# Kernel optimization log

Measured on AMD Instinct MI355X. Metric: run time of the kernel, lower is better.

## Reference

```python
import jax, jax.numpy as jnp
import numpy as np

N = 500_000
E = 5_000_000
DIM = 16
LR = 0.005
THRESHOLD = 0.0


def setup_inputs() -> dict:
    key = jax.random.key(0)
    ks = jax.random.split(key, 8)
    s = 1.0 / np.sqrt(DIM)
    return {
        "x": jax.random.normal(ks[0], (N, DIM), jnp.float32),
        "edge_index": jax.random.randint(ks[1], (2, E), 0, N, dtype=jnp.int32),
        "W1": jax.random.normal(ks[2], (DIM, DIM), jnp.float32) * s,
        "b1": jnp.zeros((DIM,), jnp.float32),
        "W2": jax.random.normal(ks[3], (DIM, DIM), jnp.float32) * s,
        "b2": jnp.zeros((DIM,), jnp.float32),
        "W3": jax.random.normal(ks[4], (DIM, DIM), jnp.float32) * s,
        "b3": jnp.zeros((DIM,), jnp.float32),
        "positive": 0,  # negative sample -> nonzero loss branch
    }


def gcn_conv(x, edge_index, W, b):
    # PyG GCNConv: h = x @ W.T, add self-loops, symmetric norm, aggregate at dst.
    n = x.shape[0]
    loop = jnp.arange(n, dtype=edge_index.dtype)
    src = jnp.concatenate([edge_index[0], loop])
    dst = jnp.concatenate([edge_index[1], loop])
    deg = jax.ops.segment_sum(jnp.ones_like(dst, x.dtype), dst, num_segments=n)
    dinv = jnp.where(deg > 0, jax.lax.rsqrt(deg), 0.0)
    norm = dinv[src] * dinv[dst]  # [E+N]
    h = x @ W.T  # [N, out]
    msg = norm[:, None] * h[src]  # irregular gather, memory-bound
    return jax.ops.segment_sum(msg, dst, num_segments=n) + b


def local_loss(g, positive):
    t = THRESHOLD
    if positive:
        return jnp.where(g > t + 10.0, 0.0,
               jnp.where(g < t - 10.0, t - g, jnp.log1p(jnp.exp(t - g))))
    return jnp.where(g > t + 10.0, t + g,
           jnp.where(g < t - 10.0, 0.0, jnp.log1p(jnp.exp(g + t))))


def reference(x, edge_index, W1, b1, W2, b2, W3, b3, positive):
    # Note: the original computes activation_normalizer(x) and loss_derivative(g)
    # into z/driv_loss but immediately overwrites both -> dead code, omitted.
    agg = jnp.float32(0.0)
    Wc, bc = W1, b1  # conv1 params, updated in-place each layer in the original
    x_cur = x
    for (W, b) in ((W1, b1), (W2, b2), (W3, b3)):
        z = jax.nn.relu(gcn_conv(x_cur, edge_index, W, b))
        goodness = jnp.sum(z * z) / z.shape[1]
        agg = agg + local_loss(goodness, positive)
        d = 2.0 * jnp.abs(z)            # activation_gradient(z)
        wd = d * d                      # weighted_deriv
        dW = x_cur.T @ wd               # [in, out]
        db = jnp.sum(wd, axis=0)
        Wc = Wc - LR * dW.T
        bc = bc - LR * db
        x_cur = z
    return agg, Wc, bc
```

## Files before the change

kernel.cpp:

```cpp
#include <hip/hip_runtime.h>
#include <math.h>

#define TPB 256
#define TPB_P 512
#define TPB_A 512
#define LRATE 0.005f

#define LOG_NPB 10
#define NPB (1 << LOG_NPB)
#define CAP 14336
#define CHUNK 4096
#define CPT (CHUNK / TPB_P)

#define NTILE 64

#define FXS  65536.0f
#define FXSI (1.0f / 65536.0f)

#if __has_builtin(__builtin_amdgcn_cvt_f32_fp8) && __has_builtin(__builtin_amdgcn_cvt_pk_fp8_f32)
__device__ __forceinline__ float fp8_dec(unsigned char v) {
    return __builtin_amdgcn_cvt_f32_fp8((int)v, 0);
}
__device__ __forceinline__ unsigned fp8_pk4(float a, float b, float c, float d) {
    int w = __builtin_amdgcn_cvt_pk_fp8_f32(a, b, 0, false);
    w = __builtin_amdgcn_cvt_pk_fp8_f32(c, d, w, true);
    return (unsigned)w;
}
#else
__device__ __forceinline__ unsigned char fp8_enc1(float f) {
    unsigned u = __float_as_uint(f);
    unsigned s = (u >> 24) & 0x80u;
    u &= 0x7FFFFFFFu;
    if (u >= 0x43E00000u) return (unsigned char)(s | 0x7E);
    if (u < 0x3C800000u) {
        float a = __uint_as_float(u);
        int m = (int)rintf(a * 512.f);
        return (unsigned char)(s | (unsigned)m);
    }
    unsigned mant = u & 0x7FFFFFu;
    unsigned rest = mant & 0xFFFFFu;
    unsigned keep = u >> 20;
    keep += (rest > 0x80000u || (rest == 0x80000u && (keep & 1u))) ? 1u : 0u;
    int eb = (int)(keep >> 3) - 127 + 7;
    return (unsigned char)(s | (unsigned)((eb << 3) | (int)(keep & 7u)));
}
__device__ __forceinline__ float fp8_dec(unsigned char v) {
    unsigned s = ((unsigned)(v & 0x80u)) << 24;
    unsigned e = (v >> 3) & 0xFu;
    unsigned m = v & 7u;
    if (e == 0) {
        float r = (float)m * 0.001953125f;
        return (v & 0x80u) ? -r : r;
    }
    return __uint_as_float(s | ((e + 120u) << 23) | (m << 20));
}
__device__ __forceinline__ unsigned fp8_pk4(float a, float b, float c, float d) {
    return (unsigned)fp8_enc1(a) | ((unsigned)fp8_enc1(b) << 8) |
           ((unsigned)fp8_enc1(c) << 16) | ((unsigned)fp8_enc1(d) << 24);
}
#endif

#if __has_builtin(__builtin_amdgcn_cvt_pk_f32_fp8)
typedef float __attribute__((ext_vector_type(2))) f32x2;
__device__ __forceinline__ void fp8_dec4(unsigned w, float& a, float& b, float& c, float& d) {
    f32x2 lo = __builtin_amdgcn_cvt_pk_f32_fp8((int)w, false);
    f32x2 hi = __builtin_amdgcn_cvt_pk_f32_fp8((int)w, true);
    a = lo[0]; b = lo[1]; c = hi[0]; d = hi[1];
}
#else
__device__ __forceinline__ void fp8_dec4(unsigned w, float& a, float& b, float& c, float& d) {
    a = fp8_dec((unsigned char)(w & 0xFFu));
    b = fp8_dec((unsigned char)((w >> 8) & 0xFFu));
    c = fp8_dec((unsigned char)((w >> 16) & 0xFFu));
    d = fp8_dec((unsigned char)((w >> 24) & 0xFFu));
}
#endif

__global__ __launch_bounds__(TPB_P) void k_partition(const int* __restrict__ src,
                                                     const int* __restrict__ dst,
                                                     int* __restrict__ bcur,
                                                     int* __restrict__ grec,
                                                     int E, int nbuck) {
    __shared__ int hist[TPB_P];
    __shared__ int sc[TPB_P];
    __shared__ int lstart[TPB_P];
    __shared__ int lcur[TPB_P];
    __shared__ int gbase[TPB_P];
    __shared__ int lbuf[CHUNK];
    __shared__ unsigned short bbuf[CHUNK];

    int t = threadIdx.x;
    int chunkBase = blockIdx.x * CHUNK;
    hist[t] = 0;
    __syncthreads();

    int myb[CPT], myrec[CPT];
#pragma unroll
    for (int k = 0; k < CPT; k++) {
        int e = chunkBase + k * TPB_P + t;
        if (e < E) {
            int d = dst[e];
            int s = src[e];
            int b = d >> LOG_NPB;
            myb[k] = b;
            myrec[k] = (s << LOG_NPB) | (d & (NPB - 1));
            atomicAdd(&hist[b], 1);
        } else myb[k] = -1;
    }
    __syncthreads();

    int c = hist[t];
    sc[t] = c;
    __syncthreads();
#pragma unroll
    for (int off = 1; off < TPB_P; off <<= 1) {
        int add = (t >= off) ? sc[t - off] : 0;
        __syncthreads();
        sc[t] += add;
        __syncthreads();
    }
    int excl = sc[t] - c;
    lstart[t] = excl;
    lcur[t] = excl;
    if (t < nbuck && c > 0) gbase[t] = atomicAdd(&bcur[t * 16], c);
    __syncthreads();

#pragma unroll
    for (int k = 0; k < CPT; k++) {
        if (myb[k] >= 0) {
            int p = atomicAdd(&lcur[myb[k]], 1);
            lbuf[p] = myrec[k];
            bbuf[p] = (unsigned short)myb[k];
        }
    }
    __syncthreads();

    int total = E - chunkBase; if (total > CHUNK) total = CHUNK;
    for (int p = t; p < total; p += TPB_P) {
        int b = (int)bbuf[p];
        int pos = gbase[b] + (p - lstart[b]);
        if (pos < CAP) grec[(size_t)b * CAP + pos] = lbuf[p];
    }
}

__global__ __launch_bounds__(TPB) void k_sort(int* __restrict__ bcur,
                                              int* __restrict__ grec,
                                              float* __restrict__ dinv, int N) {
    __shared__ int lbuf[CAP];
    __shared__ int obuf[CAP];
    __shared__ int deg[NPB];
    __shared__ int hist[NTILE];
    __shared__ int curp[NTILE];
    int t = threadIdx.x;
    int b = blockIdx.x;
    int cnt = bcur[b * 16]; if (cnt > CAP) cnt = CAP;
    const size_t base = (size_t)b * CAP;

    for (int i = t; i < NTILE; i += TPB) hist[i] = 0;
    for (int i = t; i < NPB; i += TPB) deg[i] = 0;
    __syncthreads();
    for (int i = t; i < cnt; i += TPB) {
        int r = grec[base + i];
        lbuf[i] = r;
        atomicAdd(&deg[r & (NPB - 1)], 1);
        atomicAdd(&hist[((unsigned)r) >> 23], 1);
    }
    __syncthreads();
    if (t == 0) {
        int run = 0;
#pragma unroll
        for (int k = 0; k < NTILE; k++) { int c = hist[k]; curp[k] = run; run += c; }
    }
    __syncthreads();
    for (int i = t; i < cnt; i += TPB) {
        int r = lbuf[i];
        int p = atomicAdd(&curp[((unsigned)r) >> 23], 1);
        obuf[p] = r;
    }
    __syncthreads();
    for (int i = t; i < cnt; i += TPB) grec[base + i] = obuf[i];
    int nodeBase = b << LOG_NPB;
    for (int i = t; i < NPB; i += TPB) {
        int node = nodeBase + i;
        if (node < N) dinv[node] = rsqrtf((float)(deg[i] + 1));
    }
}

__global__ __launch_bounds__(TPB) void k_h(const float* __restrict__ xc,
                                           const float* __restrict__ W,
                                           const float* __restrict__ dinv,
                                           unsigned* __restrict__ hp, int n) {
    __shared__ float sW[256];
    if (threadIdx.x < 256) sW[threadIdx.x] = W[threadIdx.x];
    __syncthreads();
    int i = blockIdx.x * blockDim.x + threadIdx.x;
    int stride = gridDim.x * blockDim.x;
    for (; i < n; i += stride) {
        float x[16];
        const float4* xr = (const float4*)(xc + (size_t)i * 16);
#pragma unroll
        for (int q = 0; q < 4; q++) {
            float4 v = xr[q];
            x[4*q+0] = v.x; x[4*q+1] = v.y; x[4*q+2] = v.z; x[4*q+3] = v.w;
        }
        float di = dinv[i];
        float hv[16];
#pragma unroll
        for (int j = 0; j < 16; j++) {
            float s = 0.f;
#pragma unroll
            for (int k = 0; k < 16; k++) s = fmaf(x[k], sW[j*16 + k], s);
            hv[j] = di * s;
        }
        uint4 w;
        w.x = fp8_pk4(hv[0],  hv[1],  hv[2],  hv[3]);
        w.y = fp8_pk4(hv[4],  hv[5],  hv[6],  hv[7]);
        w.z = fp8_pk4(hv[8],  hv[9],  hv[10], hv[11]);
        w.w = fp8_pk4(hv[12], hv[13], hv[14], hv[15]);
        ((uint4*)hp)[i] = w;
    }
}

__global__ __launch_bounds__(TPB_A, 4) void k_agg(const int* __restrict__ bcur,
                                                  const int* __restrict__ grec,
                                                  const float* __restrict__ dinv,
                                                  const unsigned* __restrict__ hp32,
                                                  const float* __restrict__ b,
                                                  const float* __restrict__ xc,
                                                  float* __restrict__ z,
                                                  float* __restrict__ partial,
                                                  int nb, int N) {
    __shared__ int accI[16 * NPB];
    int t = threadIdx.x;
    int bkt = blockIdx.x;
    int cnt = bcur[bkt * 16]; if (cnt > CAP) cnt = CAP;
    const int nodeBase = bkt << LOG_NPB;
    const size_t recBase = (size_t)bkt * CAP;

    {
        int4 zv = make_int4(0, 0, 0, 0);
        int4* a4 = (int4*)accI;
        for (int i = t; i < 16 * NPB / 4; i += TPB_A) a4[i] = zv;
    }
    __syncthreads();

    int q = t & 3;
    int gi = t >> 2;
    int j0 = q * 4;
    int base = 0;
    for (; base + 512 <= cnt; base += 512) {
        int rec[4];
#pragma unroll
        for (int u = 0; u < 4; u++) rec[u] = grec[recBase + base + u * 128 + gi];
        unsigned w[4];
#pragma unroll
        for (int u = 0; u < 4; u++)
            w[u] = hp32[(size_t)(((unsigned)rec[u]) >> LOG_NPB) * 4 + q];
#pragma unroll
        for (int u = 0; u < 4; u++) {
            int dl = rec[u] & (NPB - 1);
            float f0, f1, f2, f3;
            fp8_dec4(w[u], f0, f1, f2, f3);
            atomicAdd(&accI[(j0 + 0) * NPB + (dl ^ (j0 + 0))], (int)(f0 * FXS));
            atomicAdd(&accI[(j0 + 1) * NPB + (dl ^ (j0 + 1))], (int)(f1 * FXS));
            atomicAdd(&accI[(j0 + 2) * NPB + (dl ^ (j0 + 2))], (int)(f2 * FXS));
            atomicAdd(&accI[(j0 + 3) * NPB + (dl ^ (j0 + 3))], (int)(f3 * FXS));
        }
    }
    for (int e = base + gi; e < cnt; e += 128) {
        int rec = grec[recBase + e];
        unsigned w = hp32[(size_t)(((unsigned)rec) >> LOG_NPB) * 4 + q];
        int dl = rec & (NPB - 1);
        float f0, f1, f2, f3;
        fp8_dec4(w, f0, f1, f2, f3);
        atomicAdd(&accI[(j0 + 0) * NPB + (dl ^ (j0 + 0))], (int)(f0 * FXS));
        atomicAdd(&accI[(j0 + 1) * NPB + (dl ^ (j0 + 1))], (int)(f1 * FXS));
        atomicAdd(&accI[(j0 + 2) * NPB + (dl ^ (j0 + 2))], (int)(f2 * FXS));
        atomicAdd(&accI[(j0 + 3) * NPB + (dl ^ (j0 + 3))], (int)(f3 * FXS));
    }
    __syncthreads();

    const unsigned char* hpB = (const unsigned char*)hp32;
    int j = t & 15;
    int g0 = t >> 4;
    float bj = b[j];
    float accW[16];
#pragma unroll
    for (int k = 0; k < 16; k++) accW[k] = 0.f;
    float accB = 0.f;

    for (int i = g0; i < NPB; i += 32) {
        int node = nodeBase + i;
        if (node >= N) break;
        float sv = fp8_dec(hpB[(size_t)node * 16 + j]);
        float aj = fmaf((float)accI[j * NPB + (i ^ j)], FXSI, sv);
        float zj = fmaxf(fmaf(dinv[node], aj, bj), 0.f);
        z[(size_t)node * 16 + j] = zj;
        float wdj = 4.f * zj * zj;
        accB += wdj;
        const float4* xrow = (const float4*)(xc + (size_t)node * 16);
        float4 x0 = xrow[0], x1 = xrow[1], x2 = xrow[2], x3 = xrow[3];
        accW[0]  = fmaf(x0.x, wdj, accW[0]);  accW[1]  = fmaf(x0.y, wdj, accW[1]);
        accW[2]  = fmaf(x0.z, wdj, accW[2]);  accW[3]  = fmaf(x0.w, wdj, accW[3]);
        accW[4]  = fmaf(x1.x, wdj, accW[4]);  accW[5]  = fmaf(x1.y, wdj, accW[5]);
        accW[6]  = fmaf(x1.z, wdj, accW[6]);  accW[7]  = fmaf(x1.w, wdj, accW[7]);
        accW[8]  = fmaf(x2.x, wdj, accW[8]);  accW[9]  = fmaf(x2.y, wdj, accW[9]);
        accW[10] = fmaf(x2.z, wdj, accW[10]); accW[11] = fmaf(x2.w, wdj, accW[11]);
        accW[12] = fmaf(x3.x, wdj, accW[12]); accW[13] = fmaf(x3.y, wdj, accW[13]);
        accW[14] = fmaf(x3.z, wdj, accW[14]); accW[15] = fmaf(x3.w, wdj, accW[15]);
    }
    __syncthreads();

    float (*red)[17] = (float (*)[17])accI;
#pragma unroll
    for (int k = 0; k < 16; k++) red[t][k] = accW[k];
    red[t][16] = accB;
    __syncthreads();
    if (t < 256) {
        int kk = t >> 4;
        int jj = t & 15;
        float s = 0.f;
#pragma unroll
        for (int g = 0; g < 32; g++) s += red[g * 16 + jj][kk];
        partial[(size_t)(kk * 16 + jj) * nb + bkt] = s;
    }
    if (t < 16) {
        float sb = 0.f;
#pragma unroll
        for (int g = 0; g < 32; g++) sb += red[g * 16 + t][16];
        partial[(size_t)(256 + t) * nb + bkt] = sb;
    }
}

__global__ __launch_bounds__(TPB) void k_reduce(const float* __restrict__ partial,
                                                float* __restrict__ acc,
                                                int nb, int total) {
    int wid = (blockIdx.x * blockDim.x + threadIdx.x) >> 6;
    int lane = threadIdx.x & 63;
    if (wid >= total) return;
    const float* p = partial + (size_t)wid * nb;
    float s = 0.f;
    for (int b = lane; b < nb; b += 64) s += p[b];
#pragma unroll
    for (int off = 32; off > 0; off >>= 1) s += __shfl_down(s, off, 64);
    if (lane == 0) acc[wid] = s;
}

__device__ __forceinline__ float local_loss_f(float g, int positive) {
    const float t = 0.0f;
    if (positive) {
        if (g > t + 10.f) return 0.f;
        if (g < t - 10.f) return t - g;
        return log1pf(expf(t - g));
    } else {
        if (g > t + 10.f) return t + g;
        if (g < t - 10.f) return 0.f;
        return log1pf(expf(g + t));
    }
}

__global__ void k_final(const float* __restrict__ W1, const float* __restrict__ b1,
                        const float* __restrict__ acc, const int* __restrict__ positive,
                        float* __restrict__ outv) {
    int t = threadIdx.x;
    if (t < 256) {
        int jj = t >> 4, kk = t & 15;
        float s = 0.f;
#pragma unroll
        for (int l = 0; l < 3; l++) s += acc[l * 272 + kk * 16 + jj];
        outv[1 + t] = W1[t] - LRATE * s;
    }
    if (t < 16) {
        float s = 0.f;
#pragma unroll
        for (int l = 0; l < 3; l++) s += acc[l * 272 + 256 + t];
        outv[257 + t] = b1[t] - LRATE * s;
    }
    if (t == 0) {
        int pos = positive[0];
        float agg = 0.f;
#pragma unroll
        for (int l = 0; l < 3; l++) {
            float g = 0.f;
#pragma unroll
            for (int jj = 0; jj < 16; jj++) g += acc[l * 272 + 256 + jj];
            g *= (1.0f / 64.0f);
            agg += local_loss_f(g, pos);
        }
        outv[0] = agg;
    }
}

extern "C" void kernel_launch(void* const* d_in, const int* in_sizes, int n_in,
                              void* d_out, int out_size, void* d_ws, size_t ws_size,
                              hipStream_t stream) {
    const float* x  = (const float*)d_in[0];
    const int*   ei = (const int*)d_in[1];
    const float* W1 = (const float*)d_in[2];
    const float* b1 = (const float*)d_in[3];
    const float* W2 = (const float*)d_in[4];
    const float* b2 = (const float*)d_in[5];
    const float* W3 = (const float*)d_in[6];
    const float* b3 = (const float*)d_in[7];
    const int* positive = (const int*)d_in[8];
    float* outv = (float*)d_out;

    const int N = in_sizes[0] / 16;
    const int E = in_sizes[1] / 2;
    const int nbuck = (N + NPB - 1) >> LOG_NPB;

    char* ws = (char*)d_ws;
    size_t off = 0;
    auto carve = [&](size_t bytes) -> void* {
        void* p = ws + off;
        off = (off + bytes + 255) & ~(size_t)255;
        return p;
    };
    int*   bcur   = (int*)  carve((size_t)nbuck * 16 * 4);
    int*   grec   = (int*)  carve((size_t)nbuck * CAP * 4);
    float* dinv   = (float*)carve((size_t)N * 4);
    float* acc    = (float*)carve(3 * 272 * 4);
    float* part   = (float*)carve((size_t)3 * 272 * nbuck * 4);
    unsigned* hp  = (unsigned*)carve((size_t)N * 16);
    float* P1     = (float*)carve((size_t)N * 64);
    float* P2     = (float*)carve((size_t)N * 64);

    hipMemsetAsync(bcur, 0, (size_t)nbuck * 16 * 4, stream);

    const int* src = ei;
    const int* dst = ei + E;

    int partBlocks = (E + CHUNK - 1) / CHUNK;
    k_partition<<<partBlocks, TPB_P, 0, stream>>>(src, dst, bcur, grec, E, nbuck);
    k_sort<<<nbuck, TPB, 0, stream>>>(bcur, grec, dinv, N);

    const float* Ws[3] = {W1, W2, W3};
    const float* bss[3] = {b1, b2, b3};
    float* outs[3] = {P1, P2, P1};

    int nodeBlocks = (N + TPB - 1) / TPB;

    const float* xc = x;
    for (int l = 0; l < 3; l++) {
        k_h<<<nodeBlocks, TPB, 0, stream>>>(xc, Ws[l], dinv, hp, N);
        k_agg<<<nbuck, TPB_A, 0, stream>>>(bcur, grec, dinv, hp, bss[l],
                                           xc, outs[l],
                                           part + (size_t)l * 272 * nbuck, nbuck, N);
        xc = outs[l];
    }
    int totalElems = 3 * 272;
    k_reduce<<<(totalElems * 64 + TPB - 1) / TPB, TPB, 0, stream>>>(part, acc, nbuck, totalElems);
    k_final<<<1, 256, 0, stream>>>(W1, b1, acc, positive, outv);
}
```

Measured before the change: 389.7 us.

## Halve nodes per bucket to double bucket count and raise aggregation occupancy

Shrinks each destination bucket from 1024 to 512 nodes, which roughly doubles the bucket count to about 977. The partition kernel now handles two buckets per thread in its histogram and prefix scan. The sort kernel runs with 512 threads and shifts its tile key, and the aggregation kernel's shared accumulator shrinks, with launch bounds raised to 8 waves per SIMD. The aim is more blocks and higher occupancy in the aggregation and sort stages. The risks are more global atomics in partition, a smaller per-bucket capacity (7680) that could overflow on skewed degrees, and possible register spills under the tighter launch bounds.

```diff
diff --git a/kernel.cpp b/kernel.cpp
--- a/kernel.cpp
+++ b/kernel.cpp
@@ -6,9 +6,10 @@
 #define TPB_A 512
 #define LRATE 0.005f
 
-#define LOG_NPB 10
+#define LOG_NPB 9
 #define NPB (1 << LOG_NPB)
-#define CAP 14336
+#define NBUCK_MAX 1024
+#define CAP 7680
 #define CHUNK 4096
 #define CPT (CHUNK / TPB_P)
 
@@ -81,17 +82,18 @@
                                                      int* __restrict__ bcur,
                                                      int* __restrict__ grec,
                                                      int E, int nbuck) {
-    __shared__ int hist[TPB_P];
+    __shared__ int hist[NBUCK_MAX];
     __shared__ int sc[TPB_P];
-    __shared__ int lstart[TPB_P];
-    __shared__ int lcur[TPB_P];
-    __shared__ int gbase[TPB_P];
+    __shared__ int lstart[NBUCK_MAX];
+    __shared__ int lcur[NBUCK_MAX];
+    __shared__ int gbase[NBUCK_MAX];
     __shared__ int lbuf[CHUNK];
     __shared__ unsigned short bbuf[CHUNK];
 
     int t = threadIdx.x;
     int chunkBase = blockIdx.x * CHUNK;
     hist[t] = 0;
+    hist[t + TPB_P] = 0;
     __syncthreads();
 
     int myb[CPT], myrec[CPT];
@@ -109,7 +111,8 @@
     }
     __syncthreads();
 
-    int c = hist[t];
+    int c0 = hist[2 * t], c1 = hist[2 * t + 1];
+    int c = c0 + c1;
     sc[t] = c;
     __syncthreads();
 #pragma unroll
@@ -120,9 +123,10 @@
         __syncthreads();
     }
     int excl = sc[t] - c;
-    lstart[t] = excl;
-    lcur[t] = excl;
-    if (t < nbuck && c > 0) gbase[t] = atomicAdd(&bcur[t * 16], c);
+    lstart[2 * t] = excl;       lcur[2 * t] = excl;
+    lstart[2 * t + 1] = excl + c0; lcur[2 * t + 1] = excl + c0;
+    if (c0 > 0) gbase[2 * t]     = atomicAdd(&bcur[(2 * t) * 16], c0);
+    if (c1 > 0) gbase[2 * t + 1] = atomicAdd(&bcur[(2 * t + 1) * 16], c1);
     __syncthreads();
 
 #pragma unroll
@@ -143,9 +147,9 @@
     }
 }
 
-__global__ __launch_bounds__(TPB) void k_sort(int* __restrict__ bcur,
-                                              int* __restrict__ grec,
-                                              float* __restrict__ dinv, int N) {
+__global__ __launch_bounds__(TPB_P) void k_sort(int* __restrict__ bcur,
+                                                int* __restrict__ grec,
+                                                float* __restrict__ dinv, int N) {
     __shared__ int lbuf[CAP];
     __shared__ int obuf[CAP];
     __shared__ int deg[NPB];
@@ -156,14 +160,14 @@
     int cnt = bcur[b * 16]; if (cnt > CAP) cnt = CAP;
     const size_t base = (size_t)b * CAP;
 
-    for (int i = t; i < NTILE; i += TPB) hist[i] = 0;
-    for (int i = t; i < NPB; i += TPB) deg[i] = 0;
-    __syncthreads();
-    for (int i = t; i < cnt; i += TPB) {
+    for (int i = t; i < NTILE; i += TPB_P) hist[i] = 0;
+    for (int i = t; i < NPB; i += TPB_P) deg[i] = 0;
+    __syncthreads();
+    for (int i = t; i < cnt; i += TPB_P) {
         int r = grec[base + i];
         lbuf[i] = r;
         atomicAdd(&deg[r & (NPB - 1)], 1);
-        atomicAdd(&hist[((unsigned)r) >> 23], 1);
+        atomicAdd(&hist[((unsigned)r) >> 22], 1);
     }
     __syncthreads();
     if (t == 0) {
@@ -172,15 +176,15 @@
         for (int k = 0; k < NTILE; k++) { int c = hist[k]; curp[k] = run; run += c; }
     }
     __syncthreads();
-    for (int i = t; i < cnt; i += TPB) {
+    for (int i = t; i < cnt; i += TPB_P) {
         int r = lbuf[i];
-        int p = atomicAdd(&curp[((unsigned)r) >> 23], 1);
+        int p = atomicAdd(&curp[((unsigned)r) >> 22], 1);
         obuf[p] = r;
     }
     __syncthreads();
-    for (int i = t; i < cnt; i += TPB) grec[base + i] = obuf[i];
+    for (int i = t; i < cnt; i += TPB_P) grec[base + i] = obuf[i];
     int nodeBase = b << LOG_NPB;
-    for (int i = t; i < NPB; i += TPB) {
+    for (int i = t; i < NPB; i += TPB_P) {
         int node = nodeBase + i;
         if (node < N) dinv[node] = rsqrtf((float)(deg[i] + 1));
     }
@@ -221,7 +225,7 @@
     }
 }
 
-__global__ __launch_bounds__(TPB_A, 4) void k_agg(const int* __restrict__ bcur,
+__global__ __launch_bounds__(TPB_A, 8) void k_agg(const int* __restrict__ bcur,
                                                   const int* __restrict__ grec,
                                                   const float* __restrict__ dinv,
                                                   const unsigned* __restrict__ hp32,
@@ -230,7 +234,7 @@
                                                   float* __restrict__ z,
                                                   float* __restrict__ partial,
                                                   int nb, int N) {
-    __shared__ int accI[16 * NPB];
+    __shared__ int accI[TPB_A * 17];
     int t = threadIdx.x;
     int bkt = blockIdx.x;
     int cnt = bcur[bkt * 16]; if (cnt > CAP) cnt = CAP;
@@ -432,7 +436,7 @@
 
     int partBlocks = (E + CHUNK - 1) / CHUNK;
     k_partition<<<partBlocks, TPB_P, 0, stream>>>(src, dst, bcur, grec, E, nbuck);
-    k_sort<<<nbuck, TPB, 0, stream>>>(bcur, grec, dinv, N);
+    k_sort<<<nbuck, TPB_P, 0, stream>>>(bcur, grec, dinv, N);
 
     const float* Ws[3] = {W1, W2, W3};
     const float* bss[3] = {b1, b2, b3};
```

Measured after the change: 420.0 us. 1.08x slower.
